# Performance work log

Measured on AMD Instinct MI355X. Metric: run time of the kernel, lower is better.

## Reference

```python
import jax, jax.numpy as jnp
import numpy as np

N, E, DIN, HID, H, ED = 50000, 800000, 128, 64, 4, 5
Z_IDX = 3          # impedance column
PHYS_W = 1.0       # physics_weight
NEG_SLOPE = 0.2    # GATv2 leaky_relu slope


def gat_layer(x, src, dst, ea, Wl, bl, Wr, br, We, att, temp, bias, concat):
    """PhysicsGATv2Conv (add_self_loops=False, eval mode / no dropout)."""
    n = x.shape[0]
    Hh, C = att.shape
    xl = (x @ Wl + bl).reshape(n, Hh, C)   # lin_l -> source features
    xr = (x @ Wr + br).reshape(n, Hh, C)   # lin_r -> target features
    # physics-enhanced edge attr: overwrite last column with temp * w / |Z|
    z = jnp.clip(ea[:, Z_IDX], 1e-6, None)
    ea = ea.at[:, -1].set(temp * PHYS_W / z)
    e = (ea @ We).reshape(-1, Hh, C)       # lin_edge (no bias)
    m = jax.nn.leaky_relu(xl[src] + xr[dst] + e, NEG_SLOPE)  # [E,H,C]
    logit = jnp.einsum('ehc,hc->eh', m, att)                 # [E,H]
    # segment softmax over incoming edges of each target node
    lmax = jax.ops.segment_max(logit, dst, num_segments=n)
    w = jnp.exp(logit - lmax[dst])
    den = jax.ops.segment_sum(w, dst, num_segments=n)
    a = w / (den[dst] + 1e-16)
    out = jax.ops.segment_sum(xl[src] * a[:, :, None], dst, num_segments=n)
    out = out.reshape(n, Hh * C) if concat else out.mean(axis=1)
    return out + bias


def layer_norm(x, w, b):
    mu = x.mean(-1, keepdims=True)
    v = ((x - mu) ** 2).mean(-1, keepdims=True)
    return (x - mu) * jax.lax.rsqrt(v + 1e-5) * w + b


def setup_inputs() -> dict:
    key = jax.random.key(0)
    ks = iter(jax.random.split(key, 40))
    nk = lambda: next(ks)
    d = {}
    d['x'] = jax.random.normal(nk(), (N, DIN), jnp.float32)
    d['edge_index'] = jax.random.randint(nk(), (2, E), 0, N)
    d['edge_attr'] = jax.random.uniform(nk(), (E, ED), jnp.float32)
    hd = HID * H
    cfg = [(DIN, True), (hd, True), (hd, False)]
    for i, (din, concat) in enumerate(cfg):
        dout = hd if concat else HID
        d[f'Wl{i}'] = jax.random.normal(nk(), (din, hd), jnp.float32) / np.sqrt(din)
        d[f'bl{i}'] = 0.01 * jax.random.normal(nk(), (hd,), jnp.float32)
        d[f'Wr{i}'] = jax.random.normal(nk(), (din, hd), jnp.float32) / np.sqrt(din)
        d[f'br{i}'] = 0.01 * jax.random.normal(nk(), (hd,), jnp.float32)
        d[f'We{i}'] = jax.random.normal(nk(), (ED, hd), jnp.float32) / np.sqrt(ED)
        d[f'att{i}'] = jax.random.normal(nk(), (H, HID), jnp.float32) / np.sqrt(HID)
        d[f'temp{i}'] = jnp.float32(1.0)
        d[f'bias{i}'] = 0.01 * jax.random.normal(nk(), (dout,), jnp.float32)
        d[f'lnw{i}'] = jnp.ones((dout,), jnp.float32)
        d[f'lnb{i}'] = jnp.zeros((dout,), jnp.float32)
    d['pw0'] = jax.random.normal(nk(), (DIN, hd), jnp.float32) / np.sqrt(DIN)
    d['pb0'] = jnp.zeros((hd,), jnp.float32)
    d['pw2'] = jax.random.normal(nk(), (hd, HID), jnp.float32) / np.sqrt(hd)
    d['pb2'] = jnp.zeros((HID,), jnp.float32)
    return d


def reference(x, edge_index, edge_attr,
              Wl0, bl0, Wr0, br0, We0, att0, temp0, bias0, lnw0, lnb0,
              Wl1, bl1, Wr1, br1, We1, att1, temp1, bias1, lnw1, lnb1,
              Wl2, bl2, Wr2, br2, We2, att2, temp2, bias2, lnw2, lnb2,
              pw0, pb0, pw2, pb2):
    src, dst = edge_index[0], edge_index[1]
    # layer 0: 128 -> 256 (concat), residual projected
    h = gat_layer(x, src, dst, edge_attr, Wl0, bl0, Wr0, br0, We0, att0, temp0, bias0, True)
    h = layer_norm(h, lnw0, lnb0) + (x @ pw0 + pb0)
    h = jax.nn.elu(h)
    # layer 1: 256 -> 256 (concat), identity residual
    h1 = gat_layer(h, src, dst, edge_attr, Wl1, bl1, Wr1, br1, We1, att1, temp1, bias1, True)
    h = layer_norm(h1, lnw1, lnb1) + h
    h = jax.nn.elu(h)
    # layer 2: 256 -> 64 (head-mean), residual projected, no activation
    h2 = gat_layer(h, src, dst, edge_attr, Wl2, bl2, Wr2, br2, We2, att2, temp2, bias2, False)
    out = layer_norm(h2, lnw2, lnb2) + (h @ pw2 + pb2)
    return out
```

## Files before the change

kernel.cpp:

```cpp
#include <hip/hip_runtime.h>
#include <math.h>

#define NN 50000
#define EE 800000
#define NB 196

typedef _Float16 half8 __attribute__((ext_vector_type(8)));
typedef _Float16 hv4  __attribute__((ext_vector_type(4)));
typedef _Float16 hv2  __attribute__((ext_vector_type(2)));
typedef float floatx16 __attribute__((ext_vector_type(16)));
typedef float fv4 __attribute__((ext_vector_type(4)));

__device__ __forceinline__ float fexp2(float x) { return __builtin_amdgcn_exp2f(x); }

template<int CTRL>
__device__ __forceinline__ float dppadd(float x) {
    int t = __builtin_amdgcn_update_dpp(0, __float_as_int(x), CTRL, 0xf, 0xf, false);
    return x + __int_as_float(t);
}
__device__ __forceinline__ float red16(float x) {
    x = dppadd<0x121>(x);
    x = dppadd<0x122>(x);
    x = dppadd<0x124>(x);
    x = dppadd<0x128>(x);
    return x;
}

__global__ __launch_bounds__(256) void swizzleA(
    const float* __restrict__ A, _Float16* __restrict__ Asw, int M, int K)
{
    int wave = threadIdx.x >> 6, lane = threadIdx.x & 63;
    int tile = blockIdx.x;
    int kc = blockIdx.y * 4 + wave;
    int KC = K >> 4;
    if (kc >= KC) return;
    int row = tile * 32 + (lane & 31);
    int k0 = kc * 16 + (lane >> 5) * 8;
    float4 v0 = make_float4(0.f, 0.f, 0.f, 0.f);
    float4 v1 = make_float4(0.f, 0.f, 0.f, 0.f);
    if (row < M) {
        const float* p = A + (size_t)row * K + k0;
        v0 = *(const float4*)p;
        v1 = *(const float4*)(p + 4);
    }
    half8 o;
    o[0] = (_Float16)v0.x; o[1] = (_Float16)v0.y;
    o[2] = (_Float16)v0.z; o[3] = (_Float16)v0.w;
    o[4] = (_Float16)v1.x; o[5] = (_Float16)v1.y;
    o[6] = (_Float16)v1.z; o[7] = (_Float16)v1.w;
    *(half8*)(Asw + (((size_t)tile * KC + kc) * 64 + lane) * 8) = o;
}

__global__ __launch_bounds__(256) void prep_weights(
    const float* __restrict__ s0, const float* __restrict__ s1,
    const float* __restrict__ s2, const float* __restrict__ s3,
    const float* __restrict__ s4, const float* __restrict__ s5,
    const float* __restrict__ s6, const float* __restrict__ s7,
    _Float16* __restrict__ catB0, _Float16* __restrict__ catB1,
    _Float16* __restrict__ catB2,
    const float* __restrict__ bl0, const float* __restrict__ br0,
    const float* __restrict__ pb0, const float* __restrict__ bl1,
    const float* __restrict__ br1, const float* __restrict__ bl2,
    const float* __restrict__ br2, const float* __restrict__ pb2,
    float* __restrict__ cb0, float* __restrict__ cb1, float* __restrict__ cb2)
{
    int b = blockIdx.x;
    if (b >= 184) {
        int t = (b - 184) * 256 + threadIdx.x;
        if (t < 768) {
            cb0[t] = (t < 256) ? bl0[t] : (t < 512) ? br0[t - 256] : pb0[t - 512];
        } else if (t < 1280) {
            int u = t - 768;
            cb1[u] = (u < 256) ? bl1[u] : br1[u - 256];
        } else if (t < 1856) {
            int u = t - 1280;
            cb2[u] = (u < 256) ? bl2[u] : (u < 512) ? br2[u - 256] : pb2[u - 512];
        }
        return;
    }
    int wave = threadIdx.x >> 6, lane = threadIdx.x & 63;
    int pair = b * 4 + wave;
    const int cum[9] = {0, 64, 128, 192, 320, 448, 576, 704, 736};
    int job = 0;
    while (pair >= cum[job + 1]) ++job;
    const float* srcs[8] = {s0, s1, s2, s3, s4, s5, s6, s7};
    const int KCs[8] = {8, 8, 8, 16, 16, 16, 16, 16};
    const int NCs[8] = {256, 256, 256, 256, 256, 256, 256, 64};
    const int ntb[8] = {0, 8, 16, 0, 8, 0, 8, 16};
    _Float16* dsts[8] = {catB0, catB0, catB0, catB1, catB1, catB2, catB2, catB2};
    int p = pair - cum[job];
    int KC = KCs[job], NC = NCs[job];
    int nt = p / KC, kc = p - nt * KC;
    int n = (nt >> 1) * 64 + ((lane & 31) * 2) + (nt & 1);
    int k0 = kc * 16 + (lane >> 5) * 8;
    const float* B = srcs[job];
    half8 o;
#pragma unroll
    for (int jj = 0; jj < 8; ++jj)
        o[jj] = (_Float16)B[(size_t)(k0 + jj) * NC + n];
    int ntG = ntb[job] + nt;
    *(half8*)(dsts[job] + (((size_t)ntG * KC + kc) * 64 + lane) * 8) = o;
}

__global__ __launch_bounds__(256) void gemm_mfma(
    const _Float16* __restrict__ Asw, const _Float16* __restrict__ Bsw,
    const float* __restrict__ bias, _Float16* __restrict__ C,
    int M, int K, int NC)
{
    const int wave = threadIdx.x >> 6, lane = threadIdx.x & 63;
    const int KC = K >> 4;
    const int rt0 = blockIdx.x * 4 + (wave & 1) * 2;
    const int NG = NC >> 6;
    int g = blockIdx.y * 2 + (wave >> 1);
    if (g >= NG) g = NG - 1;

    const half8* Ap0 = (const half8*)Asw + (size_t)rt0 * KC * 64 + lane;
    const half8* Ap1 = Ap0 + (size_t)KC * 64;
    const half8* Bp0 = (const half8*)Bsw + (size_t)(2 * g) * KC * 64 + lane;
    const half8* Bp1 = Bp0 + (size_t)KC * 64;

    floatx16 accE0 = {0.f}, accE1 = {0.f}, accO0 = {0.f}, accO1 = {0.f};

#pragma unroll 4
    for (int kc = 0; kc < KC; ++kc) {
        half8 a0 = Ap0[(size_t)kc * 64];
        half8 a1 = Ap1[(size_t)kc * 64];
        half8 b0 = Bp0[(size_t)kc * 64];
        half8 b1 = Bp1[(size_t)kc * 64];
        accE0 = __builtin_amdgcn_mfma_f32_32x32x16_f16(a0, b0, accE0, 0, 0, 0);
        accE1 = __builtin_amdgcn_mfma_f32_32x32x16_f16(a1, b0, accE1, 0, 0, 0);
        accO0 = __builtin_amdgcn_mfma_f32_32x32x16_f16(a0, b1, accO0, 0, 0, 0);
        accO1 = __builtin_amdgcn_mfma_f32_32x32x16_f16(a1, b1, accO1, 0, 0, 0);
    }

    const int nlane = lane & 31, hs = lane >> 5;
    int colb = g * 64 + nlane * 2;
    float be = bias[colb], bo = bias[colb + 1];
#pragma unroll
    for (int r = 0; r < 16; ++r) {
        int rowin = (r & 3) + 8 * (r >> 2) + 4 * hs;
        int row0 = rt0 * 32 + rowin;
        int row1 = row0 + 32;
        if (row0 < M) {
            hv2 pe;
            pe[0] = (_Float16)(accE0[r] + be);
            pe[1] = (_Float16)(accO0[r] + bo);
            *(hv2*)(C + (size_t)row0 * NC + colb) = pe;
        }
        if (row1 < M) {
            hv2 po;
            po[0] = (_Float16)(accE1[r] + be);
            po[1] = (_Float16)(accO1[r] + bo);
            *(hv2*)(C + (size_t)row1 * NC + colb) = po;
        }
    }
}

__global__ __launch_bounds__(256) void hist_kernel(const int* __restrict__ dst,
                                                   int* __restrict__ deg)
{
    int e = blockIdx.x * 256 + threadIdx.x;
    if (e < EE) atomicAdd(&deg[dst[e]], 1);
}

__global__ __launch_bounds__(256) void scan_local(const int* __restrict__ deg,
                                                  int* __restrict__ rowoff,
                                                  int* __restrict__ part)
{
    __shared__ int sd[256];
    int tid = threadIdx.x;
    int i = blockIdx.x * 256 + tid;
    int v = (i < NN) ? deg[i] : 0;
    sd[tid] = v;
    __syncthreads();
    for (int off = 1; off < 256; off <<= 1) {
        int t = (tid >= off) ? sd[tid - off] : 0;
        __syncthreads();
        sd[tid] += t;
        __syncthreads();
    }
    if (i < NN) rowoff[i] = sd[tid] - v;
    if (tid == 255) part[blockIdx.x] = sd[255];
}

__global__ __launch_bounds__(256) void scan_part(int* __restrict__ part,
                                                 int* __restrict__ rowoff)
{
    __shared__ int sd[256];
    int tid = threadIdx.x;
    int v = (tid < NB) ? part[tid] : 0;
    sd[tid] = v;
    __syncthreads();
    for (int off = 1; off < 256; off <<= 1) {
        int t = (tid >= off) ? sd[tid - off] : 0;
        __syncthreads();
        sd[tid] += t;
        __syncthreads();
    }
    if (tid < NB) part[tid] = sd[tid] - v;
    if (tid == 0) rowoff[NN] = EE;
}

__global__ __launch_bounds__(256) void scan_add(int* __restrict__ rowoff,
                                                const int* __restrict__ part,
                                                int* __restrict__ cursor)
{
    int i = blockIdx.x * 256 + threadIdx.x;
    if (i < NN) {
        rowoff[i] += part[blockIdx.x];
        cursor[i] = 0;
    }
}

__global__ __launch_bounds__(256) void scatter_kernel(
    const int* __restrict__ src, const int* __restrict__ dst,
    const float* __restrict__ ea, const int* __restrict__ rowoff,
    int* __restrict__ cursor, int* __restrict__ srcp,
    float4* __restrict__ eap, float* __restrict__ erec)
{
    int e = blockIdx.x * 256 + threadIdx.x;
    if (e < EE) {
        int d = dst[e];
        int pos = rowoff[d] + atomicAdd(&cursor[d], 1);
        srcp[pos] = src[e];
        const float* p = ea + (size_t)e * 5;
        eap[pos] = make_float4(p[0], p[1], p[2], p[3]);
        erec[pos] = 1.0f / fmaxf(p[3], 1e-6f);
    }
}

template<int MODE, int RSTRIDE>
__global__ __launch_bounds__(256) void fused_attn_ln(
    const int* __restrict__ rowoff, const int* __restrict__ srcp,
    const float4* __restrict__ eap, const float* __restrict__ erec,
    const _Float16* __restrict__ xlp,
    const float* __restrict__ We, const float* __restrict__ att,
    const float* __restrict__ temp, const float* __restrict__ bias,
    const float* __restrict__ lnw, const float* __restrict__ lnb,
    const _Float16* __restrict__ residH, const float* __restrict__ residF,
    float* __restrict__ outF, _Float16* __restrict__ aswOut)
{
    int v = __builtin_amdgcn_readfirstlane(blockIdx.x * 4 + (threadIdx.x >> 6));
    int lane = threadIdx.x & 63;
    if (v >= NN) return;
    int grp = lane >> 4;
    int sub = lane & 15;
    int j = grp * 64 + sub * 4;

    fv4 ww0 = *(const fv4*)(We + j);
    fv4 ww1 = *(const fv4*)(We + 256 + j);
    fv4 ww2 = *(const fv4*)(We + 512 + j);
    fv4 ww3 = *(const fv4*)(We + 768 + j);
    fv4 ww4 = *(const fv4*)(We + 1024 + j);
    fv4 atv = *(const fv4*)(att + j);
    fv4 xrv = __builtin_convertvector(
        *(const hv4*)(xlp + (size_t)v * RSTRIDE + 256 + j), fv4);
    float tmp = temp[0];
    const float L2E = 1.44269504088896340736f;

    float mxd = -INFINITY, dend = 0.f;
    fv4 acc = {0.f, 0.f, 0.f, 0.f};

    int beg = __builtin_amdgcn_readfirstlane(rowoff[v]);
    int end = __builtin_amdgcn_readfirstlane(rowoff[v + 1]);
    int i = beg;
    for (; i + 4 <= end; i += 4) {
        int s[4]; float4 a[4]; float q[4]; fv4 xv[4]; float l[4];
#pragma unroll
        for (int u = 0; u < 4; ++u) {
            s[u] = __builtin_amdgcn_readfirstlane(srcp[i + u]);
            a[u] = eap[i + u];
            q[u] = tmp * erec[i + u];
        }
#pragma unroll
        for (int u = 0; u < 4; ++u)
            xv[u] = __builtin_convertvector(
                *(const hv4*)(xlp + (size_t)s[u] * RSTRIDE + j), fv4);
#pragma unroll
        for (int u = 0; u < 4; ++u) {
            fv4 m = xv[u] + xrv;
            m = m + a[u].x * ww0; m = m + a[u].y * ww1; m = m + a[u].z * ww2;
            m = m + a[u].w * ww3; m = m + q[u] * ww4;
            m = __builtin_elementwise_max(m, m * 0.2f);
            fv4 p = m * atv;
            l[u] = (p[0] + p[1]) + (p[2] + p[3]);
        }
#pragma unroll
        for (int u = 0; u < 4; ++u) l[u] = red16(l[u]) * L2E;
        float nm = fmaxf(fmaxf(l[0], l[1]), fmaxf(l[2], l[3]));
        nm = fmaxf(nm, mxd);
        float sc = fexp2(mxd - nm);
        float e0 = fexp2(l[0] - nm);
        float e1 = fexp2(l[1] - nm);
        float e2 = fexp2(l[2] - nm);
        float e3 = fexp2(l[3] - nm);
        mxd = nm;
        dend = dend * sc + ((e0 + e1) + (e2 + e3));
        acc = acc * sc +
              ((xv[0] * e0 + xv[1] * e1) + (xv[2] * e2 + xv[3] * e3));
    }
    for (; i < end; ++i) {
        int s0 = __builtin_amdgcn_readfirstlane(srcp[i]);
        float4 a0 = eap[i];
        float q0 = tmp * erec[i];
        fv4 x0 = __builtin_convertvector(
            *(const hv4*)(xlp + (size_t)s0 * RSTRIDE + j), fv4);
        fv4 m0 = x0 + xrv;
        m0 = m0 + a0.x * ww0; m0 = m0 + a0.y * ww1; m0 = m0 + a0.z * ww2;
        m0 = m0 + a0.w * ww3; m0 = m0 + q0 * ww4;
        m0 = __builtin_elementwise_max(m0, m0 * 0.2f);
        fv4 p0 = m0 * atv;
        float l0 = (p0[0] + p0[1]) + (p0[2] + p0[3]);
        l0 = red16(l0) * L2E;
        float nm = fmaxf(mxd, l0);
        float sc = fexp2(mxd - nm);
        float e0 = fexp2(l0 - nm);
        mxd = nm;
        dend = dend * sc + e0;
        acc = acc * sc + x0 * e0;
    }

    float inv = __builtin_amdgcn_rcpf(dend + 1e-16f);
    if (MODE <= 1) {
        fv4 bb = *(const fv4*)(bias + j);
        fv4 o = acc * inv + bb;
        float s  = (o[0] + o[1]) + (o[2] + o[3]);
        fv4 oq = o * o;
        float s2 = (oq[0] + oq[1]) + (oq[2] + oq[3]);
        s = red16(s);   s += __shfl_xor(s, 16, 64);  s += __shfl_xor(s, 32, 64);
        s2 = red16(s2); s2 += __shfl_xor(s2, 16, 64); s2 += __shfl_xor(s2, 32, 64);
        float mu = s * (1.f / 256.f);
        float var = s2 * (1.f / 256.f) - mu * mu;
        float rs = __builtin_amdgcn_rsqf(var + 1e-5f);
        fv4 lw = *(const fv4*)(lnw + j);
        fv4 lb = *(const fv4*)(lnb + j);
        fv4 rr;
        if (MODE == 0)
            rr = __builtin_convertvector(
                *(const hv4*)(residH + (size_t)v * RSTRIDE + j), fv4);
        else
            rr = *(const fv4*)(residF + (size_t)v * 256 + j);
        fv4 y = (o - mu) * rs * lw + lb + rr;
        y[0] = (y[0] > 0.f) ? y[0] : fexp2(y[0] * L2E) - 1.f;
        y[1] = (y[1] > 0.f) ? y[1] : fexp2(y[1] * L2E) - 1.f;
        y[2] = (y[2] > 0.f) ? y[2] : fexp2(y[2] * L2E) - 1.f;
        y[3] = (y[3] > 0.f) ? y[3] : fexp2(y[3] * L2E) - 1.f;
        if (MODE == 0)
            *(fv4*)(outF + (size_t)v * 256 + j) = y;
        int kc = j >> 4, half = (j >> 3) & 1, off = j & 7;
        size_t idx = (((size_t)(v >> 5) * 16 + kc) * 64 + (v & 31) + 32 * half) * 8 + off;
        hv4 yh = __builtin_convertvector(y, hv4);
        *(hv4*)(aswOut + idx) = yh;
    } else {
        fv4 r = acc * inv;
        r[0] += __shfl_xor(r[0], 16, 64); r[0] += __shfl_xor(r[0], 32, 64);
        r[1] += __shfl_xor(r[1], 16, 64); r[1] += __shfl_xor(r[1], 32, 64);
        r[2] += __shfl_xor(r[2], 16, 64); r[2] += __shfl_xor(r[2], 32, 64);
        r[3] += __shfl_xor(r[3], 16, 64); r[3] += __shfl_xor(r[3], 32, 64);
        fv4 bb = *(const fv4*)(bias + sub * 4);
        fv4 o = r * 0.25f + bb;
        float s  = (o[0] + o[1]) + (o[2] + o[3]);
        fv4 oq = o * o;
        float s2 = (oq[0] + oq[1]) + (oq[2] + oq[3]);
        s = red16(s);
        s2 = red16(s2);
        float mu = s * (1.f / 64.f);
        float var = s2 * (1.f / 64.f) - mu * mu;
        float rs = __builtin_amdgcn_rsqf(var + 1e-5f);
        fv4 lw = *(const fv4*)(lnw + sub * 4);
        fv4 lb = *(const fv4*)(lnb + sub * 4);
        fv4 rr = __builtin_convertvector(
            *(const hv4*)(residH + (size_t)v * RSTRIDE + sub * 4), fv4);
        fv4 y = (o - mu) * rs * lw + lb + rr;
        if (grp == 0)
            *(fv4*)(outF + (size_t)v * 64 + sub * 4) = y;
    }
}

extern "C" void kernel_launch(void* const* d_in, const int* in_sizes, int n_in,
                              void* d_out, int out_size, void* d_ws, size_t ws_size,
                              hipStream_t stream)
{
    const float* x    = (const float*)d_in[0];
    const int*   eidx = (const int*)d_in[1];
    const float* ea   = (const float*)d_in[2];
    const int* src = eidx;
    const int* dst = eidx + EE;

    const float *Wl[3], *bl[3], *Wr[3], *br[3], *We[3], *att[3], *temp[3],
                *bias[3], *lnw[3], *lnb[3];
    for (int i = 0; i < 3; ++i) {
        int b = 3 + i * 10;
        Wl[i]   = (const float*)d_in[b + 0];
        bl[i]   = (const float*)d_in[b + 1];
        Wr[i]   = (const float*)d_in[b + 2];
        br[i]   = (const float*)d_in[b + 3];
        We[i]   = (const float*)d_in[b + 4];
        att[i]  = (const float*)d_in[b + 5];
        temp[i] = (const float*)d_in[b + 6];
        bias[i] = (const float*)d_in[b + 7];
        lnw[i]  = (const float*)d_in[b + 8];
        lnb[i]  = (const float*)d_in[b + 9];
    }
    const float* pw0 = (const float*)d_in[33];
    const float* pb0 = (const float*)d_in[34];
    const float* pw2 = (const float*)d_in[35];
    const float* pb2 = (const float*)d_in[36];

    char* w = (char*)d_ws;
    float* h     = (float*)w; w += (size_t)NN * 256 * 4;
    char*  gbase = w;         w += (size_t)NN * 256 * 4;
    _Float16* xlr = (_Float16*)w; w += (size_t)NN * 768 * 2;
    float4* eap  = (float4*)w; w += (size_t)EE * 16;
    float* erec  = (float*)w; w += (size_t)EE * 4;
    int* srcp    = (int*)w;   w += (size_t)EE * 4;
    int* rowoff  = (int*)w;   w += (size_t)(NN + 16) * 4;
    int* cursor  = (int*)w;   w += (size_t)NN * 4;
    int* part    = (int*)w;   w += 1024;
    w = (char*)(((uintptr_t)w + 255) & ~(uintptr_t)255);
    _Float16* catB0 = (_Float16*)w; w += 196608;
    _Float16* catB1 = (_Float16*)w; w += 262144;
    _Float16* catB2 = (_Float16*)w; w += 294912;
    float* cb0 = (float*)w; w += 768 * 4;
    float* cb1 = (float*)w; w += 512 * 4;
    float* cb2 = (float*)w; w += 576 * 4;
    _Float16* Asw = (_Float16*)gbase;

    dim3 blk(256);
    dim3 grid_e((EE + 255) / 256);
    dim3 grid_nw((NN + 3) / 4);
    dim3 grid_nb(NB);
    const int MT = 391;

    hipMemsetAsync(cursor, 0, (size_t)NN * 4, stream);
    hipLaunchKernelGGL(hist_kernel, grid_e, blk, 0, stream, dst, cursor);
    hipLaunchKernelGGL(scan_local, grid_nb, blk, 0, stream, cursor, rowoff, part);
    hipLaunchKernelGGL(scan_part, dim3(1), blk, 0, stream, part, rowoff);
    hipLaunchKernelGGL(scan_add, grid_nb, blk, 0, stream, rowoff, part, cursor);
    hipLaunchKernelGGL(scatter_kernel, grid_e, blk, 0, stream,
                       src, dst, ea, rowoff, cursor, srcp, eap, erec);

    hipLaunchKernelGGL(prep_weights, dim3(192), blk, 0, stream,
                       Wl[0], Wr[0], pw0, Wl[1], Wr[1], Wl[2], Wr[2], pw2,
                       catB0, catB1, catB2,
                       bl[0], br[0], pb0, bl[1], br[1], bl[2], br[2], pb2,
                       cb0, cb1, cb2);

    swizzleA<<<dim3(1564, 2), blk, 0, stream>>>(x, Asw, NN, 128);
    gemm_mfma<<<dim3(MT, 6), blk, 0, stream>>>(
        Asw, catB0, cb0, xlr, NN, 128, 768);
    fused_attn_ln<0, 768><<<grid_nw, blk, 0, stream>>>(
        rowoff, srcp, eap, erec, xlr, We[0], att[0], temp[0],
        bias[0], lnw[0], lnb[0], xlr + 512, nullptr, h, Asw);

    gemm_mfma<<<dim3(MT, 4), blk, 0, stream>>>(
        Asw, catB1, cb1, xlr, NN, 256, 512);
    fused_attn_ln<1, 512><<<grid_nw, blk, 0, stream>>>(
        rowoff, srcp, eap, erec, xlr, We[1], att[1], temp[1],
        bias[1], lnw[1], lnb[1], nullptr, h, nullptr, Asw);

    gemm_mfma<<<dim3(MT, 5), blk, 0, stream>>>(
        Asw, catB2, cb2, xlr, NN, 256, 576);
    fused_attn_ln<2, 576><<<grid_nw, blk, 0, stream>>>(
        rowoff, srcp, eap, erec, xlr, We[2], att[2], temp[2],
        bias[2], lnw[2], lnb[2], xlr + 512, nullptr, (float*)d_out, nullptr);
}
```

Before: 635.4 us.

## Make attention kernel persistent and pack src index with reciprocal impedance

```diff
diff --git a/kernel.cpp b/kernel.cpp
--- a/kernel.cpp
+++ b/kernel.cpp
@@ -4,6 +4,7 @@
 #define NN 50000
 #define EE 800000
 #define NB 196
+#define TOTW 8192
 
 typedef _Float16 half8 __attribute__((ext_vector_type(8)));
 typedef _Float16 hv4  __attribute__((ext_vector_type(4)));
@@ -215,24 +216,24 @@
 __global__ __launch_bounds__(256) void scatter_kernel(
     const int* __restrict__ src, const int* __restrict__ dst,
     const float* __restrict__ ea, const int* __restrict__ rowoff,
-    int* __restrict__ cursor, int* __restrict__ srcp,
-    float4* __restrict__ eap, float* __restrict__ erec)
+    int* __restrict__ cursor, int2* __restrict__ sre,
+    float4* __restrict__ eap)
 {
     int e = blockIdx.x * 256 + threadIdx.x;
     if (e < EE) {
         int d = dst[e];
         int pos = rowoff[d] + atomicAdd(&cursor[d], 1);
-        srcp[pos] = src[e];
         const float* p = ea + (size_t)e * 5;
         eap[pos] = make_float4(p[0], p[1], p[2], p[3]);
-        erec[pos] = 1.0f / fmaxf(p[3], 1e-6f);
+        float rc = 1.0f / fmaxf(p[3], 1e-6f);
+        sre[pos] = make_int2(src[e], __float_as_int(rc));
     }
 }
 
 template<int MODE, int RSTRIDE>
 __global__ __launch_bounds__(256) void fused_attn_ln(
-    const int* __restrict__ rowoff, const int* __restrict__ srcp,
-    const float4* __restrict__ eap, const float* __restrict__ erec,
+    const int* __restrict__ rowoff, const int2* __restrict__ sre,
+    const float4* __restrict__ eap,
     const _Float16* __restrict__ xlp,
     const float* __restrict__ We, const float* __restrict__ att,
     const float* __restrict__ temp, const float* __restrict__ bias,
@@ -240,9 +241,8 @@
     const _Float16* __restrict__ residH, const float* __restrict__ residF,
     float* __restrict__ outF, _Float16* __restrict__ aswOut)
 {
-    int v = __builtin_amdgcn_readfirstlane(blockIdx.x * 4 + (threadIdx.x >> 6));
+    int wid = blockIdx.x * 4 + (threadIdx.x >> 6);
     int lane = threadIdx.x & 63;
-    if (v >= NN) return;
     int grp = lane >> 4;
     int sub = lane & 15;
     int j = grp * 64 + sub * 4;
@@ -251,129 +251,132 @@
     fv4 ww1 = *(const fv4*)(We + 256 + j);
     fv4 ww2 = *(const fv4*)(We + 512 + j);
     fv4 ww3 = *(const fv4*)(We + 768 + j);
-    fv4 ww4 = *(const fv4*)(We + 1024 + j);
+    fv4 ww4 = *(const fv4*)(We + 1024 + j) * temp[0];
     fv4 atv = *(const fv4*)(att + j);
-    fv4 xrv = __builtin_convertvector(
-        *(const hv4*)(xlp + (size_t)v * RSTRIDE + 256 + j), fv4);
-    float tmp = temp[0];
+    const int jb = (MODE == 2) ? sub * 4 : j;
+    fv4 bb = *(const fv4*)(bias + jb);
+    fv4 lw = *(const fv4*)(lnw + jb);
+    fv4 lb = *(const fv4*)(lnb + jb);
     const float L2E = 1.44269504088896340736f;
 
-    float mxd = -INFINITY, dend = 0.f;
-    fv4 acc = {0.f, 0.f, 0.f, 0.f};
-
-    int beg = __builtin_amdgcn_readfirstlane(rowoff[v]);
-    int end = __builtin_amdgcn_readfirstlane(rowoff[v + 1]);
-    int i = beg;
-    for (; i + 4 <= end; i += 4) {
-        int s[4]; float4 a[4]; float q[4]; fv4 xv[4]; float l[4];
-#pragma unroll
-        for (int u = 0; u < 4; ++u) {
-            s[u] = __builtin_amdgcn_readfirstlane(srcp[i + u]);
-            a[u] = eap[i + u];
-            q[u] = tmp * erec[i + u];
-        }
-#pragma unroll
-        for (int u = 0; u < 4; ++u)
-            xv[u] = __builtin_convertvector(
-                *(const hv4*)(xlp + (size_t)s[u] * RSTRIDE + j), fv4);
-#pragma unroll
-        for (int u = 0; u < 4; ++u) {
-            fv4 m = xv[u] + xrv;
-            m = m + a[u].x * ww0; m = m + a[u].y * ww1; m = m + a[u].z * ww2;
-            m = m + a[u].w * ww3; m = m + q[u] * ww4;
-            m = __builtin_elementwise_max(m, m * 0.2f);
-            fv4 p = m * atv;
-            l[u] = (p[0] + p[1]) + (p[2] + p[3]);
-        }
-#pragma unroll
-        for (int u = 0; u < 4; ++u) l[u] = red16(l[u]) * L2E;
-        float nm = fmaxf(fmaxf(l[0], l[1]), fmaxf(l[2], l[3]));
-        nm = fmaxf(nm, mxd);
-        float sc = fexp2(mxd - nm);
-        float e0 = fexp2(l[0] - nm);
-        float e1 = fexp2(l[1] - nm);
-        float e2 = fexp2(l[2] - nm);
-        float e3 = fexp2(l[3] - nm);
-        mxd = nm;
-        dend = dend * sc + ((e0 + e1) + (e2 + e3));
-        acc = acc * sc +
-              ((xv[0] * e0 + xv[1] * e1) + (xv[2] * e2 + xv[3] * e3));
-    }
-    for (; i < end; ++i) {
-        int s0 = __builtin_amdgcn_readfirstlane(srcp[i]);
-        float4 a0 = eap[i];
-        float q0 = tmp * erec[i];
-        fv4 x0 = __builtin_convertvector(
-            *(const hv4*)(xlp + (size_t)s0 * RSTRIDE + j), fv4);
-        fv4 m0 = x0 + xrv;
-        m0 = m0 + a0.x * ww0; m0 = m0 + a0.y * ww1; m0 = m0 + a0.z * ww2;
-        m0 = m0 + a0.w * ww3; m0 = m0 + q0 * ww4;
-        m0 = __builtin_elementwise_max(m0, m0 * 0.2f);
-        fv4 p0 = m0 * atv;
-        float l0 = (p0[0] + p0[1]) + (p0[2] + p0[3]);
-        l0 = red16(l0) * L2E;
-        float nm = fmaxf(mxd, l0);
-        float sc = fexp2(mxd - nm);
-        float e0 = fexp2(l0 - nm);
-        mxd = nm;
-        dend = dend * sc + e0;
-        acc = acc * sc + x0 * e0;
-    }
-
-    float inv = __builtin_amdgcn_rcpf(dend + 1e-16f);
-    if (MODE <= 1) {
-        fv4 bb = *(const fv4*)(bias + j);
-        fv4 o = acc * inv + bb;
-        float s  = (o[0] + o[1]) + (o[2] + o[3]);
-        fv4 oq = o * o;
-        float s2 = (oq[0] + oq[1]) + (oq[2] + oq[3]);
-        s = red16(s);   s += __shfl_xor(s, 16, 64);  s += __shfl_xor(s, 32, 64);
-        s2 = red16(s2); s2 += __shfl_xor(s2, 16, 64); s2 += __shfl_xor(s2, 32, 64);
-        float mu = s * (1.f / 256.f);
-        float var = s2 * (1.f / 256.f) - mu * mu;
-        float rs = __builtin_amdgcn_rsqf(var + 1e-5f);
-        fv4 lw = *(const fv4*)(lnw + j);
-        fv4 lb = *(const fv4*)(lnb + j);
-        fv4 rr;
-        if (MODE == 0)
-            rr = __builtin_convertvector(
-                *(const hv4*)(residH + (size_t)v * RSTRIDE + j), fv4);
-        else
-            rr = *(const fv4*)(residF + (size_t)v * 256 + j);
-        fv4 y = (o - mu) * rs * lw + lb + rr;
-        y[0] = (y[0] > 0.f) ? y[0] : fexp2(y[0] * L2E) - 1.f;
-        y[1] = (y[1] > 0.f) ? y[1] : fexp2(y[1] * L2E) - 1.f;
-        y[2] = (y[2] > 0.f) ? y[2] : fexp2(y[2] * L2E) - 1.f;
-        y[3] = (y[3] > 0.f) ? y[3] : fexp2(y[3] * L2E) - 1.f;
-        if (MODE == 0)
-            *(fv4*)(outF + (size_t)v * 256 + j) = y;
-        int kc = j >> 4, half = (j >> 3) & 1, off = j & 7;
-        size_t idx = (((size_t)(v >> 5) * 16 + kc) * 64 + (v & 31) + 32 * half) * 8 + off;
-        hv4 yh = __builtin_convertvector(y, hv4);
-        *(hv4*)(aswOut + idx) = yh;
-    } else {
-        fv4 r = acc * inv;
-        r[0] += __shfl_xor(r[0], 16, 64); r[0] += __shfl_xor(r[0], 32, 64);
-        r[1] += __shfl_xor(r[1], 16, 64); r[1] += __shfl_xor(r[1], 32, 64);
-        r[2] += __shfl_xor(r[2], 16, 64); r[2] += __shfl_xor(r[2], 32, 64);
-        r[3] += __shfl_xor(r[3], 16, 64); r[3] += __shfl_xor(r[3], 32, 64);
-        fv4 bb = *(const fv4*)(bias + sub * 4);
-        fv4 o = r * 0.25f + bb;
-        float s  = (o[0] + o[1]) + (o[2] + o[3]);
-        fv4 oq = o * o;
-        float s2 = (oq[0] + oq[1]) + (oq[2] + oq[3]);
-        s = red16(s);
-        s2 = red16(s2);
-        float mu = s * (1.f / 64.f);
-        float var = s2 * (1.f / 64.f) - mu * mu;
-        float rs = __builtin_amdgcn_rsqf(var + 1e-5f);
-        fv4 lw = *(const fv4*)(lnw + sub * 4);
-        fv4 lb = *(const fv4*)(lnb + sub * 4);
-        fv4 rr = __builtin_convertvector(
-            *(const hv4*)(residH + (size_t)v * RSTRIDE + sub * 4), fv4);
-        fv4 y = (o - mu) * rs * lw + lb + rr;
-        if (grp == 0)
-            *(fv4*)(outF + (size_t)v * 64 + sub * 4) = y;
+    for (int vv = wid; vv < NN; vv += TOTW) {
+        int v = __builtin_amdgcn_readfirstlane(vv);
+        fv4 xrv = __builtin_convertvector(
+            *(const hv4*)(xlp + (size_t)v * RSTRIDE + 256 + j), fv4);
+
+        float mxd = -INFINITY, dend = 0.f;
+        fv4 acc = {0.f, 0.f, 0.f, 0.f};
+
+        int beg = __builtin_amdgcn_readfirstlane(rowoff[v]);
+        int end = __builtin_amdgcn_readfirstlane(rowoff[v + 1]);
+        int i = beg;
+        for (; i + 4 <= end; i += 4) {
+            int s[4]; float4 a[4]; float q[4]; fv4 xv[4]; float l[4];
+#pragma unroll
+            for (int u = 0; u < 4; ++u) {
+                int2 se = sre[i + u];
+                s[u] = __builtin_amdgcn_readfirstlane(se.x);
+                q[u] = __int_as_float(se.y);
+                a[u] = eap[i + u];
+            }
+#pragma unroll
+            for (int u = 0; u < 4; ++u)
+                xv[u] = __builtin_convertvector(
+                    *(const hv4*)(xlp + (size_t)s[u] * RSTRIDE + j), fv4);
+#pragma unroll
+            for (int u = 0; u < 4; ++u) {
+                fv4 m = xv[u] + xrv;
+                m = m + a[u].x * ww0; m = m + a[u].y * ww1; m = m + a[u].z * ww2;
+                m = m + a[u].w * ww3; m = m + q[u] * ww4;
+                m = __builtin_elementwise_max(m, m * 0.2f);
+                fv4 p = m * atv;
+                l[u] = (p[0] + p[1]) + (p[2] + p[3]);
+            }
+#pragma unroll
+            for (int u = 0; u < 4; ++u) l[u] = red16(l[u]) * L2E;
+            float nm = fmaxf(fmaxf(l[0], l[1]), fmaxf(l[2], l[3]));
+            nm = fmaxf(nm, mxd);
+            float sc = fexp2(mxd - nm);
+            float e0 = fexp2(l[0] - nm);
+            float e1 = fexp2(l[1] - nm);
+            float e2 = fexp2(l[2] - nm);
+            float e3 = fexp2(l[3] - nm);
+            mxd = nm;
+            dend = dend * sc + ((e0 + e1) + (e2 + e3));
+            acc = acc * sc +
+                  ((xv[0] * e0 + xv[1] * e1) + (xv[2] * e2 + xv[3] * e3));
+        }
+        for (; i < end; ++i) {
+            int2 se = sre[i];
+            int s0 = __builtin_amdgcn_readfirstlane(se.x);
+            float q0 = __int_as_float(se.y);
+            float4 a0 = eap[i];
+            fv4 x0 = __builtin_convertvector(
+                *(const hv4*)(xlp + (size_t)s0 * RSTRIDE + j), fv4);
+            fv4 m0 = x0 + xrv;
+            m0 = m0 + a0.x * ww0; m0 = m0 + a0.y * ww1; m0 = m0 + a0.z * ww2;
+            m0 = m0 + a0.w * ww3; m0 = m0 + q0 * ww4;
+            m0 = __builtin_elementwise_max(m0, m0 * 0.2f);
+            fv4 p0 = m0 * atv;
+            float l0 = (p0[0] + p0[1]) + (p0[2] + p0[3]);
+            l0 = red16(l0) * L2E;
+            float nm = fmaxf(mxd, l0);
+            float sc = fexp2(mxd - nm);
+            float e0 = fexp2(l0 - nm);
+            mxd = nm;
+            dend = dend * sc + e0;
+            acc = acc * sc + x0 * e0;
+        }
+
+        float inv = __builtin_amdgcn_rcpf(dend + 1e-16f);
+        if (MODE <= 1) {
+            fv4 o = acc * inv + bb;
+            float s  = (o[0] + o[1]) + (o[2] + o[3]);
+            fv4 oq = o * o;
+            float s2 = (oq[0] + oq[1]) + (oq[2] + oq[3]);
+            s = red16(s);   s += __shfl_xor(s, 16, 64);  s += __shfl_xor(s, 32, 64);
+            s2 = red16(s2); s2 += __shfl_xor(s2, 16, 64); s2 += __shfl_xor(s2, 32, 64);
+            float mu = s * (1.f / 256.f);
+            float var = s2 * (1.f / 256.f) - mu * mu;
+            float rs = __builtin_amdgcn_rsqf(var + 1e-5f);
+            fv4 rr;
+            if (MODE == 0)
+                rr = __builtin_convertvector(
+                    *(const hv4*)(residH + (size_t)v * RSTRIDE + j), fv4);
+            else
+                rr = *(const fv4*)(residF + (size_t)v * 256 + j);
+            fv4 y = (o - mu) * rs * lw + lb + rr;
+            y[0] = (y[0] > 0.f) ? y[0] : fexp2(y[0] * L2E) - 1.f;
+            y[1] = (y[1] > 0.f) ? y[1] : fexp2(y[1] * L2E) - 1.f;
+            y[2] = (y[2] > 0.f) ? y[2] : fexp2(y[2] * L2E) - 1.f;
+            y[3] = (y[3] > 0.f) ? y[3] : fexp2(y[3] * L2E) - 1.f;
+            if (MODE == 0)
+                *(fv4*)(outF + (size_t)v * 256 + j) = y;
+            int kc = j >> 4, half = (j >> 3) & 1, off = j & 7;
+            size_t idx = (((size_t)(v >> 5) * 16 + kc) * 64 + (v & 31) + 32 * half) * 8 + off;
+            hv4 yh = __builtin_convertvector(y, hv4);
+            *(hv4*)(aswOut + idx) = yh;
+        } else {
+            fv4 r = acc * inv;
+            r[0] += __shfl_xor(r[0], 16, 64); r[0] += __shfl_xor(r[0], 32, 64);
+            r[1] += __shfl_xor(r[1], 16, 64); r[1] += __shfl_xor(r[1], 32, 64);
+            r[2] += __shfl_xor(r[2], 16, 64); r[2] += __shfl_xor(r[2], 32, 64);
+            r[3] += __shfl_xor(r[3], 16, 64); r[3] += __shfl_xor(r[3], 32, 64);
+            fv4 o = r * 0.25f + bb;
+            float s  = (o[0] + o[1]) + (o[2] + o[3]);
+            fv4 oq = o * o;
+            float s2 = (oq[0] + oq[1]) + (oq[2] + oq[3]);
+            s = red16(s);
+            s2 = red16(s2);
+            float mu = s * (1.f / 64.f);
+            float var = s2 * (1.f / 64.f) - mu * mu;
+            float rs = __builtin_amdgcn_rsqf(var + 1e-5f);
+            fv4 rr = __builtin_convertvector(
+                *(const hv4*)(residH + (size_t)v * RSTRIDE + sub * 4), fv4);
+            fv4 y = (o - mu) * rs * lw + lb + rr;
+            if (grp == 0)
+                *(fv4*)(outF + (size_t)v * 64 + sub * 4) = y;
+        }
     }
 }
 
@@ -412,8 +415,7 @@
     char*  gbase = w;         w += (size_t)NN * 256 * 4;
     _Float16* xlr = (_Float16*)w; w += (size_t)NN * 768 * 2;
     float4* eap  = (float4*)w; w += (size_t)EE * 16;
-    float* erec  = (float*)w; w += (size_t)EE * 4;
-    int* srcp    = (int*)w;   w += (size_t)EE * 4;
+    int2* sre    = (int2*)w;  w += (size_t)EE * 8;
     int* rowoff  = (int*)w;   w += (size_t)(NN + 16) * 4;
     int* cursor  = (int*)w;   w += (size_t)NN * 4;
     int* part    = (int*)w;   w += 1024;
@@ -428,7 +430,7 @@
 
     dim3 blk(256);
     dim3 grid_e((EE + 255) / 256);
-    dim3 grid_nw((NN + 3) / 4);
+    dim3 grid_attn(TOTW / 4);
     dim3 grid_nb(NB);
     const int MT = 391;
 
@@ -438,7 +440,7 @@
     hipLaunchKernelGGL(scan_part, dim3(1), blk, 0, stream, part, rowoff);
     hipLaunchKernelGGL(scan_add, grid_nb, blk, 0, stream, rowoff, part, cursor);
     hipLaunchKernelGGL(scatter_kernel, grid_e, blk, 0, stream,
-                       src, dst, ea, rowoff, cursor, srcp, eap, erec);
+                       src, dst, ea, rowoff, cursor, sre, eap);
 
     hipLaunchKernelGGL(prep_weights, dim3(192), blk, 0, stream,
                        Wl[0], Wr[0], pw0, Wl[1], Wr[1], Wl[2], Wr[2], pw2,
@@ -449,19 +451,19 @@
     swizzleA<<<dim3(1564, 2), blk, 0, stream>>>(x, Asw, NN, 128);
     gemm_mfma<<<dim3(MT, 6), blk, 0, stream>>>(
         Asw, catB0, cb0, xlr, NN, 128, 768);
-    fused_attn_ln<0, 768><<<grid_nw, blk, 0, stream>>>(
-        rowoff, srcp, eap, erec, xlr, We[0], att[0], temp[0],
+    fused_attn_ln<0, 768><<<grid_attn, blk, 0, stream>>>(
+        rowoff, sre, eap, xlr, We[0], att[0], temp[0],
         bias[0], lnw[0], lnb[0], xlr + 512, nullptr, h, Asw);
 
     gemm_mfma<<<dim3(MT, 4), blk, 0, stream>>>(
         Asw, catB1, cb1, xlr, NN, 256, 512);
-    fused_attn_ln<1, 512><<<grid_nw, blk, 0, stream>>>(
-        rowoff, srcp, eap, erec, xlr, We[1], att[1], temp[1],
+    fused_attn_ln<1, 512><<<grid_attn, blk, 0, stream>>>(
+        rowoff, sre, eap, xlr, We[1], att[1], temp[1],
         bias[1], lnw[1], lnb[1], nullptr, h, nullptr, Asw);
 
     gemm_mfma<<<dim3(MT, 5), blk, 0, stream>>>(
         Asw, catB2, cb2, xlr, NN, 256, 576);
-    fused_attn_ln<2, 576><<<grid_nw, blk, 0, stream>>>(
-        rowoff, srcp, eap, erec, xlr, We[2], att[2], temp[2],
+    fused_attn_ln<2, 576><<<grid_attn, blk, 0, stream>>>(
+        rowoff, sre, eap, xlr, We[2], att[2], temp[2],
         bias[2], lnw[2], lnb[2], xlr + 512, nullptr, (float*)d_out, nullptr);
 }
```

Result: slower. 680.2 us (+7.1%).
